# Kernel tuning notes

Hardware: AMD Instinct MI355X
Metric: run time of the kernel (lower is better)

Reference implementation:

```python
import jax, jax.numpy as jnp
import numpy as np

COMMITMENT = 0.25
EPS = 1e-10


def setup_inputs() -> dict:
    key = jax.random.key(0)
    k1, k2 = jax.random.split(key)
    x = jax.random.normal(k1, (16, 16384, 64), dtype=jnp.float32)
    embed = jax.random.normal(k2, (64, 512), dtype=jnp.float32)  # [embed_dim, n_embed]
    sigma = jnp.ones((1,), dtype=jnp.float32)
    return {"x": x, "embed": embed, "sigma": sigma}


def reference(x, embed, sigma):
    # x: [B, T, D]; embed: [D, K]; sigma: [1]
    D, K = embed.shape
    flat = x.reshape(-1, D)  # [N, D]
    dist = (jnp.sum(flat * flat, axis=1, keepdims=True)
            - 2.0 * (flat @ embed)
            + jnp.sum(embed * embed, axis=0, keepdims=True))
    soft_assign = jax.nn.softmax(-sigma * dist, axis=1)  # [N, K]
    likelihoods = jnp.mean(soft_assign, axis=0)          # [K]
    embed_ind = jnp.argmax(soft_assign, axis=1)          # [N]
    hard = jnp.take(embed.T, embed_ind, axis=0)          # [N, D] gather of codewords
    soft_proj = soft_assign @ embed.T                    # [N, D]
    # straight-through: forward = hard, backward = soft path
    quantize = (soft_proj + jax.lax.stop_gradient(hard - soft_proj)).reshape(x.shape)
    # KL(uniform || likelihoods.detach()), batchmean over K, scaled by commitment
    p = 1.0 / K
    ql = jax.lax.stop_gradient(likelihoods)
    quant_loss = COMMITMENT * jnp.mean(p * (jnp.log(p) - jnp.log(ql + EPS)))
    return quantize, quant_loss, likelihoods
```

## Files before the change

kernel.cpp:

```cpp
#include <hip/hip_runtime.h>

#define NROWS    262144
#define DIMS     64
#define KCODES   512
#define MTILE    32
#define RPW      4
#define CHUNK    256
#define NCHUNK   2
#define D_PER    16
#define D_CHUNKS 4
#define NTHREADS 512

typedef int v8i __attribute__((ext_vector_type(8)));

__device__ __forceinline__ float dpp_xor1(float v) {
    int i = __builtin_amdgcn_update_dpp(0, __float_as_int(v), 0xB1, 0xF, 0xF, true);
    return __int_as_float(i);
}
__device__ __forceinline__ float dpp_xor2(float v) {
    int i = __builtin_amdgcn_update_dpp(0, __float_as_int(v), 0x4E, 0xF, 0xF, true);
    return __int_as_float(i);
}

__global__ void prep_kernel(const float* __restrict__ embed,
                            float* __restrict__ embedT,
                            float* __restrict__ enorm,
                            float* __restrict__ lik) {
    int k = blockIdx.x;
    int d = threadIdx.x;
    float v = embed[d * KCODES + k];
    embedT[k * DIMS + d] = v;
    float sq = __fmul_rn(v, v);
    int j = d & 7;
    float r = __shfl(sq, j, 64);
#pragma unroll
    for (int i = 1; i < 8; ++i)
        r = __fadd_rn(r, __shfl(sq, j + 8 * i, 64));
    float t;
    t = __shfl_xor(r, 1, 64); r = __fadd_rn(r, t);
    t = __shfl_xor(r, 2, 64); r = __fadd_rn(r, t);
    t = __shfl_xor(r, 4, 64); r = __fadd_rn(r, t);
    if (d == 0) { enorm[k] = r; lik[k] = 0.0f; }
}

__launch_bounds__(NTHREADS)
__global__ void main_kernel(const float* __restrict__ x,
                            const float* __restrict__ embed,
                            const float* __restrict__ sigma,
                            const float* __restrict__ embedT,
                            const float* __restrict__ enorm,
                            float* __restrict__ lik,
                            float* __restrict__ out) {
    __shared__ float red_lds[NTHREADS];

    const int tid = threadIdx.x;
    const int cg  = tid & 63;
    const int rg  = tid >> 6;
    const int rowbase = blockIdx.x * MTILE + rg * RPW;

    const float sigma_v = sigma[0];

    float acc[NCHUNK][RPW][4];
#pragma unroll
    for (int c = 0; c < NCHUNK; ++c)
#pragma unroll
        for (int r = 0; r < RPW; ++r)
#pragma unroll
            for (int q = 0; q < 4; ++q) acc[c][r][q] = 0.0f;

    const float4* __restrict__ eg4 = reinterpret_cast<const float4*>(embed);

    const int rg_s = __builtin_amdgcn_readfirstlane(rg);
    const float* xwave = x + (size_t)(blockIdx.x * MTILE + rg_s * RPW) * DIMS;

    for (int dc = 0; dc < D_CHUNKS; ++dc) {
#pragma unroll
        for (int ph = 0; ph < 2; ++ph) {
            const float* p0 = xwave + 0 * DIMS + dc * D_PER + ph * 8;
            const float* p1 = xwave + 1 * DIMS + dc * D_PER + ph * 8;
            const float* p2 = xwave + 2 * DIMS + dc * D_PER + ph * 8;
            const float* p3 = xwave + 3 * DIMS + dc * D_PER + ph * 8;
            v8i xs0, xs1, xs2, xs3;
            asm volatile("s_load_dwordx8 %0, %4, 0\n\t"
                         "s_load_dwordx8 %1, %5, 0\n\t"
                         "s_load_dwordx8 %2, %6, 0\n\t"
                         "s_load_dwordx8 %3, %7, 0\n\t"
                         "s_waitcnt lgkmcnt(0)"
                         : "=&s"(xs0), "=&s"(xs1), "=&s"(xs2), "=&s"(xs3)
                         : "s"(p0), "s"(p1), "s"(p2), "s"(p3));

#pragma unroll
            for (int d2l = 0; d2l < 4; ++d2l) {
                const int d2  = ph * 4 + d2l;
                const int dlo = dc * D_PER + 2 * d2;
                float4 e0a = eg4[(size_t)(dlo + 0) * 128 +  0 + cg];
                float4 e1a = eg4[(size_t)(dlo + 1) * 128 +  0 + cg];
                float4 e0b = eg4[(size_t)(dlo + 0) * 128 + 64 + cg];
                float4 e1b = eg4[(size_t)(dlo + 1) * 128 + 64 + cg];

#define ROW_FMA(r, xs)                                                        \
                {                                                             \
                    float xlo = __int_as_float(xs[2 * d2l]);                  \
                    float xhi = __int_as_float(xs[2 * d2l + 1]);              \
                    acc[0][r][0] = fmaf(xlo, e0a.x, acc[0][r][0]);            \
                    acc[0][r][1] = fmaf(xlo, e0a.y, acc[0][r][1]);            \
                    acc[0][r][2] = fmaf(xlo, e0a.z, acc[0][r][2]);            \
                    acc[0][r][3] = fmaf(xlo, e0a.w, acc[0][r][3]);            \
                    acc[0][r][0] = fmaf(xhi, e1a.x, acc[0][r][0]);            \
                    acc[0][r][1] = fmaf(xhi, e1a.y, acc[0][r][1]);            \
                    acc[0][r][2] = fmaf(xhi, e1a.z, acc[0][r][2]);            \
                    acc[0][r][3] = fmaf(xhi, e1a.w, acc[0][r][3]);            \
                    acc[1][r][0] = fmaf(xlo, e0b.x, acc[1][r][0]);            \
                    acc[1][r][1] = fmaf(xlo, e0b.y, acc[1][r][1]);            \
                    acc[1][r][2] = fmaf(xlo, e0b.z, acc[1][r][2]);            \
                    acc[1][r][3] = fmaf(xlo, e0b.w, acc[1][r][3]);            \
                    acc[1][r][0] = fmaf(xhi, e1b.x, acc[1][r][0]);            \
                    acc[1][r][1] = fmaf(xhi, e1b.y, acc[1][r][1]);            \
                    acc[1][r][2] = fmaf(xhi, e1b.z, acc[1][r][2]);            \
                    acc[1][r][3] = fmaf(xhi, e1b.w, acc[1][r][3]);            \
                }
                ROW_FMA(0, xs0)
                ROW_FMA(1, xs1)
                ROW_FMA(2, xs2)
                ROW_FMA(3, xs3)
#undef ROW_FMA
            }
        }
    }

    const int r_l = (cg >> 3) & 3;
    const int j_l = cg & 7;
    float xr;
    {
        const float* xp = x + (size_t)(rowbase + r_l) * DIMS + j_l;
        float v0 = xp[0];
        float s = __fmul_rn(v0, v0);
#pragma unroll
        for (int i = 1; i < 8; ++i) {
            float v = xp[8 * i];
            s = __fadd_rn(s, __fmul_rn(v, v));
        }
        xr = s;
    }
    {
        float t;
        t = dpp_xor1(xr);          xr = __fadd_rn(xr, t);
        t = dpp_xor2(xr);          xr = __fadd_rn(xr, t);
        t = __shfl_xor(xr, 4, 64); xr = __fadd_rn(xr, t);
    }

    float en[NCHUNK][4];
#pragma unroll
    for (int c = 0; c < NCHUNK; ++c)
#pragma unroll
        for (int q = 0; q < 4; ++q)
            en[c][q] = enorm[c * CHUNK + cg * 4 + q];

    float likpart[NCHUNK][4];
#pragma unroll
    for (int c = 0; c < NCHUNK; ++c)
#pragma unroll
        for (int q = 0; q < 4; ++q) likpart[c][q] = 0.0f;

#pragma unroll
    for (int r = 0; r < RPW; ++r) {
        float xn = __shfl(xr, r * 8, 64);
        float m = -INFINITY;
#pragma unroll
        for (int c = 0; c < NCHUNK; ++c)
#pragma unroll
            for (int q = 0; q < 4; ++q) {
                float dot  = acc[c][r][q];
                float td   = __fsub_rn(xn, __fmul_rn(2.0f, dot));
                float dist = __fadd_rn(td, en[c][q]);
                float zz   = __fmul_rn(-sigma_v, dist);
                acc[c][r][q] = zz;
                m = fmaxf(m, zz);
            }
        m = fmaxf(m, dpp_xor1(m));
        m = fmaxf(m, dpp_xor2(m));
        m = fmaxf(m, __shfl_xor(m,  4, 64));
        m = fmaxf(m, __shfl_xor(m,  8, 64));
        m = fmaxf(m, __shfl_xor(m, 16, 64));
        m = fmaxf(m, __shfl_xor(m, 32, 64));

        float s = 0.0f;
        int lcol = 1024;
#pragma unroll
        for (int c = 0; c < NCHUNK; ++c)
#pragma unroll
            for (int q = 0; q < 4; ++q) {
                float ee = expf(__fsub_rn(acc[c][r][q], m));
                acc[c][r][q] = ee;
                s += ee;
                int col = c * CHUNK + cg * 4 + q;
                lcol = (ee == 1.0f) ? min(lcol, col) : lcol;
            }
        unsigned long long b0 = __ballot(lcol < CHUNK);
        unsigned long long ba = __ballot(lcol < 1024);
        int srcl = (int)(b0 ? __ffsll(b0) : __ffsll(ba)) - 1;
        int bc = __shfl(lcol, srcl, 64);

        s = __fadd_rn(s, dpp_xor1(s));
        s = __fadd_rn(s, dpp_xor2(s));
        s = __fadd_rn(s, __shfl_xor(s,  4, 64));
        s = __fadd_rn(s, __shfl_xor(s,  8, 64));
        s = __fadd_rn(s, __shfl_xor(s, 16, 64));
        s = __fadd_rn(s, __shfl_xor(s, 32, 64));

        float invS = 1.0f / s;
#pragma unroll
        for (int c = 0; c < NCHUNK; ++c)
#pragma unroll
            for (int q = 0; q < 4; ++q)
                likpart[c][q] = fmaf(acc[c][r][q], invS, likpart[c][q]);

        int row = rowbase + r;
        __builtin_nontemporal_store(embedT[bc * DIMS + cg],
                                    &out[(size_t)row * DIMS + cg]);
    }

    red_lds[tid] = 0.0f;
    __syncthreads();
#pragma unroll
    for (int c = 0; c < NCHUNK; ++c)
#pragma unroll
        for (int q = 0; q < 4; ++q)
            atomicAdd(&red_lds[c * CHUNK + cg * 4 + q], likpart[c][q]);
    __syncthreads();
    atomicAdd(&lik[tid], red_lds[tid]);
}

__global__ void finish_kernel(const float* __restrict__ lik,
                              float* __restrict__ out) {
    int tid = threadIdx.x;
    float l = lik[tid] / 262144.0f;
    out[16777217 + tid] = l;
    const float p = 1.0f / 512.0f;
    float term = __fmul_rn(p, __fsub_rn(logf(p), logf(l + 1e-10f)));
#pragma unroll
    for (int mask = 1; mask < 64; mask <<= 1)
        term += __shfl_xor(term, mask, 64);
    __shared__ float ws[8];
    if ((tid & 63) == 0) ws[tid >> 6] = term;
    __syncthreads();
    if (tid == 0) {
        float ssum = 0.0f;
        for (int i = 0; i < 8; ++i) ssum += ws[i];
        out[16777216] = 0.25f * (ssum / 512.0f);
    }
}

extern "C" void kernel_launch(void* const* d_in, const int* in_sizes, int n_in,
                              void* d_out, int out_size, void* d_ws, size_t ws_size,
                              hipStream_t stream) {
    const float* x     = (const float*)d_in[0];
    const float* embed = (const float*)d_in[1];
    const float* sigma = (const float*)d_in[2];
    float* out = (float*)d_out;
    float* ws  = (float*)d_ws;

    float* embedT = ws;
    float* enorm  = ws + 32768;
    float* lik    = ws + 33280;

    prep_kernel<<<KCODES, DIMS, 0, stream>>>(embed, embedT, enorm, lik);
    main_kernel<<<NROWS / MTILE, NTHREADS, 0, stream>>>(x, embed, sigma,
                                                        embedT, enorm, lik, out);
    finish_kernel<<<1, NTHREADS, 0, stream>>>(lik, out);
}
```

Before: 463.2 us.

## Double rows per wave to reuse each codebook load across eight rows

Raises the row tile from 32 to 64 rows per block and from 4 to 8 rows per wave, so each float4 codebook load is reused across eight rows' FMAs instead of four. The x rows are fetched with eight scalar loads from one base pointer using immediate offsets, and the codebook pointer is advanced incrementally. This cuts global/L2 codebook traffic per FLOP and halves the grid size, at the cost of doubled accumulator registers and more SGPRs, which may lower occupancy. The row-norm lane mapping is widened to cover the eight rows.

```diff
diff --git a/kernel.cpp b/kernel.cpp
--- a/kernel.cpp
+++ b/kernel.cpp
@@ -3,8 +3,8 @@
 #define NROWS    262144
 #define DIMS     64
 #define KCODES   512
-#define MTILE    32
-#define RPW      4
+#define MTILE    64
+#define RPW      8
 #define CHUNK    256
 #define NCHUNK   2
 #define D_PER    16
@@ -76,27 +76,28 @@
     for (int dc = 0; dc < D_CHUNKS; ++dc) {
 #pragma unroll
         for (int ph = 0; ph < 2; ++ph) {
-            const float* p0 = xwave + 0 * DIMS + dc * D_PER + ph * 8;
-            const float* p1 = xwave + 1 * DIMS + dc * D_PER + ph * 8;
-            const float* p2 = xwave + 2 * DIMS + dc * D_PER + ph * 8;
-            const float* p3 = xwave + 3 * DIMS + dc * D_PER + ph * 8;
-            v8i xs0, xs1, xs2, xs3;
-            asm volatile("s_load_dwordx8 %0, %4, 0\n\t"
-                         "s_load_dwordx8 %1, %5, 0\n\t"
-                         "s_load_dwordx8 %2, %6, 0\n\t"
-                         "s_load_dwordx8 %3, %7, 0\n\t"
+            const float* px = xwave + dc * D_PER + ph * 8;
+            v8i xs0, xs1, xs2, xs3, xs4, xs5, xs6, xs7;
+            asm volatile("s_load_dwordx8 %0, %8, 0\n\t"
+                         "s_load_dwordx8 %1, %8, 256\n\t"
+                         "s_load_dwordx8 %2, %8, 512\n\t"
+                         "s_load_dwordx8 %3, %8, 768\n\t"
+                         "s_load_dwordx8 %4, %8, 1024\n\t"
+                         "s_load_dwordx8 %5, %8, 1280\n\t"
+                         "s_load_dwordx8 %6, %8, 1536\n\t"
+                         "s_load_dwordx8 %7, %8, 1792\n\t"
                          "s_waitcnt lgkmcnt(0)"
-                         : "=&s"(xs0), "=&s"(xs1), "=&s"(xs2), "=&s"(xs3)
-                         : "s"(p0), "s"(p1), "s"(p2), "s"(p3));
-
+                         : "=&s"(xs0), "=&s"(xs1), "=&s"(xs2), "=&s"(xs3),
+                           "=&s"(xs4), "=&s"(xs5), "=&s"(xs6), "=&s"(xs7)
+                         : "s"(px));
+
+            const float4* ep = eg4 + (size_t)(dc * D_PER + ph * 8) * 128;
 #pragma unroll
             for (int d2l = 0; d2l < 4; ++d2l) {
-                const int d2  = ph * 4 + d2l;
-                const int dlo = dc * D_PER + 2 * d2;
-                float4 e0a = eg4[(size_t)(dlo + 0) * 128 +  0 + cg];
-                float4 e1a = eg4[(size_t)(dlo + 1) * 128 +  0 + cg];
-                float4 e0b = eg4[(size_t)(dlo + 0) * 128 + 64 + cg];
-                float4 e1b = eg4[(size_t)(dlo + 1) * 128 + 64 + cg];
+                float4 e0a = ep[cg];
+                float4 e1a = ep[cg + 128];
+                float4 e0b = ep[cg + 64];
+                float4 e1b = ep[cg + 192];
 
 #define ROW_FMA(r, xs)                                                        \
                 {                                                             \
@@ -123,12 +124,17 @@
                 ROW_FMA(1, xs1)
                 ROW_FMA(2, xs2)
                 ROW_FMA(3, xs3)
+                ROW_FMA(4, xs4)
+                ROW_FMA(5, xs5)
+                ROW_FMA(6, xs6)
+                ROW_FMA(7, xs7)
 #undef ROW_FMA
+                ep += 256;
             }
         }
     }
 
-    const int r_l = (cg >> 3) & 3;
+    const int r_l = cg >> 3;
     const int j_l = cg & 7;
     float xr;
     {
```

After: 574.5 us. 24.0% more time.
